# Kernel tuning notes

Hardware: AMD Instinct MI355X
Metric: run time of the kernel (lower is better)

## Reference

```python
import jax, jax.numpy as jnp
import numpy as np

# MLA dims (DeepSeek-V2-Lite-class)
B, S, D = 2, 2048, 2048
H = 16
NOPE, ROPE, VD = 128, 64, 128   # qk_nope_head_dim, qk_rope_head_dim, v_head_dim
KV_RANK, Q_RANK = 512, 1536
EPS = 1e-6
THETA = 10000.0


def setup_inputs() -> dict:
    key = jax.random.key(0)
    ks = jax.random.split(key, 8)

    def init(k, shape, fan_in):
        return jax.random.normal(k, shape, jnp.float32) * (fan_in ** -0.5)

    return {
        "x": jax.random.normal(ks[0], (B, S, D), jnp.float32),
        "w_dq": init(ks[1], (D, Q_RANK), D),
        "q_a_norm": jnp.ones((Q_RANK,), jnp.float32),
        "w_uq": init(ks[2], (Q_RANK, H * (NOPE + ROPE)), Q_RANK),
        "w_dkv": init(ks[3], (D, KV_RANK + ROPE), D),
        "kv_a_norm": jnp.ones((KV_RANK,), jnp.float32),
        "w_ukv": init(ks[4], (KV_RANK, H * (NOPE + VD)), KV_RANK),
        "w_o": init(ks[5], (H * VD, D), H * VD),
    }


def _rmsnorm(x, w):
    return x * jax.lax.rsqrt(jnp.mean(x * x, axis=-1, keepdims=True) + EPS) * w


def _rope(x):
    # x: [B, S, H', d] -> rotary on last dim (half-split style)
    d = x.shape[-1]
    inv = 1.0 / (THETA ** (jnp.arange(0, d, 2, dtype=jnp.float32) / d))
    ang = jnp.arange(x.shape[1], dtype=jnp.float32)[:, None] * inv[None, :]  # [S, d/2]
    cos = jnp.cos(ang)[None, :, None, :]
    sin = jnp.sin(ang)[None, :, None, :]
    x1, x2 = jnp.split(x, 2, axis=-1)
    return jnp.concatenate([x1 * cos - x2 * sin, x2 * cos + x1 * sin], axis=-1)


def reference(x, w_dq, q_a_norm, w_uq, w_dkv, kv_a_norm, w_ukv, w_o):
    # --- low-rank Q projection ---
    q = _rmsnorm(x @ w_dq, q_a_norm) @ w_uq          # [B,S,H*(NOPE+ROPE)]
    q = q.reshape(B, S, H, NOPE + ROPE)
    q_nope, q_pe = q[..., :NOPE], q[..., NOPE:]

    # --- latent (compressed) KV projection + shared decoupled-RoPE key ---
    ckv = x @ w_dkv                                   # [B,S,KV_RANK+ROPE]
    c_kv, k_pe = ckv[..., :KV_RANK], ckv[..., KV_RANK:]
    kv = (_rmsnorm(c_kv, kv_a_norm) @ w_ukv).reshape(B, S, H, NOPE + VD)
    k_nope, v = kv[..., :NOPE], kv[..., NOPE:]

    # --- decoupled RoPE on rope dims only ---
    q_pe = _rope(q_pe)                                # [B,S,H,ROPE]
    k_pe = _rope(k_pe[:, :, None, :])                 # [B,S,1,ROPE] shared across heads

    qf = jnp.concatenate([q_nope, q_pe], axis=-1)     # [B,S,H,NOPE+ROPE]
    kf = jnp.concatenate([k_nope, jnp.broadcast_to(k_pe, (B, S, H, ROPE))], axis=-1)

    # --- scaled dot-product attention with causal mask ---
    scale = 1.0 / jnp.sqrt(jnp.float32(NOPE + ROPE))
    scores = jnp.einsum("bqhd,bkhd->bhqk", qf * scale, kf)  # [B,H,S,S]
    causal = jnp.tril(jnp.ones((S, S), bool))
    scores = jnp.where(causal[None, None], scores, -1e9)
    w = jax.nn.softmax(scores, axis=-1)
    o = jnp.einsum("bhqk,bkhd->bqhd", w, v).reshape(B, S, H * VD)
    return o @ w_o                                    # [B,S,D]
```

## Files before the change

### kernel.cpp

```cpp
#include <hip/hip_runtime.h>
#include <hip/hip_bf16.h>
#include <math.h>

#define BB 2
#define SS 2048
#define DDIM 2048
#define HH 16
#define NOPE 128
#define ROPE_D 64
#define VD 128
#define KVR 512
#define QR 1536
#define EPSF 1e-6f
#define THETA 10000.0f
#define MR (BB*SS)

typedef unsigned short u16;
typedef unsigned int u32;
typedef __attribute__((ext_vector_type(8))) short bf8_t;
typedef __attribute__((ext_vector_type(4))) float f4_t;

__device__ inline u16 f2b(float f) {
    __hip_bfloat16 h = __float2bfloat16(f);
    return __builtin_bit_cast(u16, h);
}

#define GLD16(g, l) __builtin_amdgcn_global_load_lds( \
    (const __attribute__((address_space(1))) u32*)(g), \
    (__attribute__((address_space(3))) u32*)(l), 16, 0, 0)

#define MFMA16(a,b,c) __builtin_amdgcn_mfma_f32_16x16x32_bf16((a),(b),(c),0,0,0)

__device__ inline void cstore(float* p, float v) { *p = v; }
__device__ inline void cstore(u16* p, float v)   { *p = f2b(v); }

__global__ void cvt_bf16_k(const float* __restrict__ in, u16* __restrict__ out, int n4) {
    int i = blockIdx.x * 256 + threadIdx.x;
    if (i < n4) {
        float4 v = ((const float4*)in)[i];
        u16* o = out + (size_t)i * 4;
        o[0] = f2b(v.x); o[1] = f2b(v.y); o[2] = f2b(v.z); o[3] = f2b(v.w);
    }
}

__global__ void transpose_bf16_k(const float* __restrict__ W, u16* __restrict__ WT,
                                 int K, int N, int Npad) {
    __shared__ float t[32][33];
    int n0 = blockIdx.x * 32, k0 = blockIdx.y * 32;
    int tx = threadIdx.x, ty = threadIdx.y;
    for (int i = ty; i < 32; i += 8) {
        int n = n0 + tx;
        t[i][tx] = (n < N) ? W[(size_t)(k0 + i) * N + n] : 0.f;
    }
    __syncthreads();
    for (int i = ty; i < 32; i += 8) {
        int n = n0 + i;
        if (n < Npad) WT[(size_t)n * K + k0 + tx] = f2b(t[tx][i]);
    }
}

template <typename TO>
__global__ __launch_bounds__(256, 2)
void gemm_mfma(const u16* __restrict__ A, const u16* __restrict__ BT,
               TO* __restrict__ C, int K, int Nreal) {
    __shared__ u16 lA[128 * 32];
    __shared__ u16 lB[128 * 32];
    const int tid = threadIdx.x;
    const int w = tid >> 6, lane = tid & 63;
    const int quad = lane >> 4, col = lane & 15;
    const int wm = (w >> 1) * 64, wn = (w & 1) * 64;
    const int bm = blockIdx.y * 128, bn = blockIdx.x * 128;
    const int srow = lane >> 2;
    const int scol = (lane & 3) * 8;
    f4_t acc[4][4] = {};
    for (int k0 = 0; k0 < K; k0 += 32) {
        __syncthreads();
        #pragma unroll
        for (int cc = 0; cc < 2; cc++) {
            int c = 2 * w + cc;
            int row = c * 16 + srow;
            GLD16(A  + (size_t)(bm + row) * K + k0 + scol, (char*)lA + c * 1024);
            GLD16(BT + (size_t)(bn + row) * K + k0 + scol, (char*)lB + c * 1024);
        }
        __syncthreads();
        bf8_t af[4], bf[4];
        #pragma unroll
        for (int i = 0; i < 4; i++) {
            af[i] = *(const bf8_t*)(lA + (wm + i * 16 + col) * 32 + quad * 8);
            bf[i] = *(const bf8_t*)(lB + (wn + i * 16 + col) * 32 + quad * 8);
        }
        #pragma unroll
        for (int mi = 0; mi < 4; mi++)
            #pragma unroll
            for (int ni = 0; ni < 4; ni++)
                acc[mi][ni] = MFMA16(af[mi], bf[ni], acc[mi][ni]);
    }
    #pragma unroll
    for (int mi = 0; mi < 4; mi++)
        #pragma unroll
        for (int ni = 0; ni < 4; ni++) {
            int n = bn + wn + ni * 16 + col;
            if (n < Nreal) {
                #pragma unroll
                for (int r = 0; r < 4; r++) {
                    int m = bm + wm + mi * 16 + quad * 4 + r;
                    cstore(C + (size_t)m * Nreal + n, acc[mi][ni][r]);
                }
            }
        }
}

__global__ void rmsnorm_bf16_k(const float* __restrict__ in, int istride, int ncols,
                               const float* __restrict__ wt, u16* __restrict__ out, int ostride) {
    __shared__ float red[256];
    int row = blockIdx.x, tid = threadIdx.x;
    const float* rp = in + (size_t)row * istride;
    float s = 0.f;
    for (int c = tid; c < ncols; c += 256) { float v = rp[c]; s += v * v; }
    red[tid] = s;
    __syncthreads();
    for (int off = 128; off > 0; off >>= 1) {
        if (tid < off) red[tid] += red[tid + off];
        __syncthreads();
    }
    float sc = rsqrtf(red[0] / (float)ncols + EPSF);
    u16* op = out + (size_t)row * ostride;
    for (int c = tid; c < ncols; c += 256) op[c] = f2b(rp[c] * sc * wt[c]);
}

__global__ void rope_q_k(const float* __restrict__ q, u16* __restrict__ qb) {
    int idx = blockIdx.x;
    int pos = (idx >> 4) & (SS - 1);
    const float* src = q + (size_t)idx * 192;
    u16* dst = qb + (size_t)idx * 192;
    int t = threadIdx.x;
    dst[t]      = f2b(src[t]);
    dst[t + 64] = f2b(src[t + 64]);
    if (t < 32) {
        float inv = powf(THETA, -(float)t * (1.0f / 32.0f));
        float ang = (float)pos * inv;
        float cs, sn; sincosf(ang, &sn, &cs);
        float x1 = src[128 + t], x2 = src[160 + t];
        dst[128 + t] = f2b(x1 * cs - x2 * sn);
        dst[160 + t] = f2b(x2 * cs + x1 * sn);
    }
}

__global__ void rope_kpe_k(const float* __restrict__ ckv, u16* __restrict__ kpe) {
    int row = blockIdx.x;
    int pos = row & (SS - 1);
    int t = threadIdx.x;
    float inv = powf(THETA, -(float)t * (1.0f / 32.0f));
    float ang = (float)pos * inv;
    float cs, sn; sincosf(ang, &sn, &cs);
    const float* pe = ckv + (size_t)row * 576 + 512;
    float x1 = pe[t], x2 = pe[t + 32];
    kpe[(size_t)row * 64 + t]      = f2b(x1 * cs - x2 * sn);
    kpe[(size_t)row * 64 + 32 + t] = f2b(x2 * cs + x1 * sn);
}

__global__ __launch_bounds__(256, 2)
void attn_mfma(const u16* __restrict__ qb, const u16* __restrict__ kvb,
               const u16* __restrict__ kpe, u16* __restrict__ ob) {
    __shared__ u16 lK[64 * 200];
    __shared__ u16 lV[128 * 72];
    __shared__ u16 lP[4 * 16 * 72];
    const int tid = threadIdx.x, w = tid >> 6, lane = tid & 63;
    const int quad = lane >> 4, col = lane & 15;
    const int bh = blockIdx.x, b = bh >> 4, h = bh & 15;
    const int qt = 31 - (int)blockIdx.y;
    const int tok0 = b * SS;
    bf8_t qf[6];
    {
        int qtok = tok0 + qt * 64 + w * 16 + col;
        const u16* qp = qb + ((size_t)qtok * HH + h) * 192 + quad * 8;
        #pragma unroll
        for (int kc = 0; kc < 6; kc++) qf[kc] = *(const bf8_t*)(qp + kc * 32);
    }
    f4_t o[8] = {};
    float mrow[4] = {-1e30f, -1e30f, -1e30f, -1e30f};
    float lrow[4] = {0.f, 0.f, 0.f, 0.f};
    const float SCL = 0.07216878364870322f * 1.4426950408889634f;
    u16* pw = lP + w * 16 * 72;
    for (int kt = 0; kt <= qt; kt++) {
        int ktok = tok0 + kt * 64;
        __syncthreads();
        for (int c = w; c < 25; c += 4) {
            int o_b = c * 1024 + lane * 16;
            int row = o_b / 400;
            int ro  = o_b - row * 400;
            const u16* src;
            if (ro < 256)      src = kvb + ((size_t)(ktok + row) * HH + h) * 256 + (ro >> 1);
            else if (ro < 384) src = kpe + (size_t)(ktok + row) * 64 + ((ro - 256) >> 1);
            else               src = kpe;
            GLD16(src, (char*)lK + c * 1024);
        }
        #pragma unroll
        for (int i = 0; i < 4; i++) {
            int dv8 = w + i * 4;
            const u16* vp = kvb + ((size_t)(ktok + lane) * HH + h) * 256 + 128 + dv8 * 8;
            bf8_t vv = *(const bf8_t*)vp;
            #pragma unroll
            for (int j = 0; j < 8; j++) lV[(dv8 * 8 + j) * 72 + lane] = (u16)vv[j];
        }
        __syncthreads();
        f4_t s[4] = {};
        #pragma unroll
        for (int kc = 0; kc < 6; kc++) {
            #pragma unroll
            for (int t = 0; t < 4; t++) {
                bf8_t kf = *(const bf8_t*)(lK + (t * 16 + col) * 200 + kc * 32 + quad * 8);
                s[t] = MFMA16(qf[kc], kf, s[t]);
            }
        }
        float sm[4] = {-1e30f, -1e30f, -1e30f, -1e30f};
        #pragma unroll
        for (int t = 0; t < 4; t++) {
            int kg = kt * 64 + t * 16 + col;
            #pragma unroll
            for (int r = 0; r < 4; r++) {
                int qg = qt * 64 + w * 16 + quad * 4 + r;
                float v = (kg <= qg) ? s[t][r] * SCL : -1e30f;
                s[t][r] = v;
                sm[r] = fmaxf(sm[r], v);
            }
        }
        #pragma unroll
        for (int off = 1; off < 16; off <<= 1)
            #pragma unroll
            for (int r = 0; r < 4; r++) sm[r] = fmaxf(sm[r], __shfl_xor(sm[r], off));
        float al[4];
        #pragma unroll
        for (int r = 0; r < 4; r++) {
            float mn = fmaxf(mrow[r], sm[r]);
            al[r] = exp2f(mrow[r] - mn);
            mrow[r] = mn;
        }
        float rs[4] = {0.f, 0.f, 0.f, 0.f};
        #pragma unroll
        for (int t = 0; t < 4; t++)
            #pragma unroll
            for (int r = 0; r < 4; r++) {
                float p = exp2f(s[t][r] - mrow[r]);
                s[t][r] = p;
                rs[r] += p;
            }
        #pragma unroll
        for (int off = 1; off < 16; off <<= 1)
            #pragma unroll
            for (int r = 0; r < 4; r++) rs[r] += __shfl_xor(rs[r], off);
        #pragma unroll
        for (int r = 0; r < 4; r++) lrow[r] = lrow[r] * al[r] + rs[r];
        #pragma unroll
        for (int n = 0; n < 8; n++)
            #pragma unroll
            for (int r = 0; r < 4; r++) o[n][r] *= al[r];
        #pragma unroll
        for (int t = 0; t < 4; t++)
            #pragma unroll
            for (int r = 0; r < 4; r++)
                pw[(quad * 4 + r) * 72 + t * 16 + col] = f2b(s[t][r]);
        #pragma unroll
        for (int kc2 = 0; kc2 < 2; kc2++) {
            bf8_t pf = *(const bf8_t*)(pw + col * 72 + kc2 * 32 + quad * 8);
            #pragma unroll
            for (int n = 0; n < 8; n++) {
                bf8_t vf = *(const bf8_t*)(lV + (n * 16 + col) * 72 + kc2 * 32 + quad * 8);
                o[n] = MFMA16(pf, vf, o[n]);
            }
        }
    }
    #pragma unroll
    for (int n = 0; n < 8; n++)
        #pragma unroll
        for (int r = 0; r < 4; r++) {
            int qtok = tok0 + qt * 64 + w * 16 + quad * 4 + r;
            float v = o[n][r] / lrow[r];
            ob[((size_t)qtok * HH + h) * 128 + n * 16 + col] = f2b(v);
        }
}

extern "C" void kernel_launch(void* const* d_in, const int* in_sizes, int n_in,
                              void* d_out, int out_size, void* d_ws, size_t ws_size,
                              hipStream_t stream) {
    const float* x        = (const float*)d_in[0];
    const float* w_dq     = (const float*)d_in[1];
    const float* q_a_norm = (const float*)d_in[2];
    const float* w_uq     = (const float*)d_in[3];
    const float* w_dkv    = (const float*)d_in[4];
    const float* kv_a_nrm = (const float*)d_in[5];
    const float* w_ukv    = (const float*)d_in[6];
    const float* w_o      = (const float*)d_in[7];
    float* out = (float*)d_out;

    char* ws = (char*)d_ws;
    const size_t MB = 1024 * 1024;
    u16*   xb    = (u16*)(ws);
    u16*   wT    = (u16*)(ws + 16 * MB);
    float* qlat  = (float*)(ws + 25 * MB);
    u16*   qlb   = (u16*)(ws + 49 * MB);
    float* qf32  = (float*)(ws + 61 * MB);
    u16*   qbuf  = (u16*)(ws + 25 * MB);
    float* ckv   = (float*)(ws + 49 * MB);
    u16*   ckvnb = (u16*)(ws + 61 * MB);
    u16*   kpeb  = (u16*)(ws + 61 * MB + 4 * MB);
    u16*   kvb   = (u16*)(ws + 61 * MB + 5 * MB);
    u16*   aob   = (u16*)(ws);

    cvt_bf16_k<<<(MR * DDIM / 4 + 255) / 256, 256, 0, stream>>>(x, xb, MR * DDIM / 4);
    transpose_bf16_k<<<dim3(1536 / 32, 2048 / 32), dim3(32, 8), 0, stream>>>(w_dq, wT, 2048, 1536, 1536);
    gemm_mfma<float><<<dim3(1536 / 128, MR / 128), 256, 0, stream>>>(xb, wT, qlat, 2048, 1536);
    rmsnorm_bf16_k<<<MR, 256, 0, stream>>>(qlat, QR, QR, q_a_norm, qlb, QR);
    transpose_bf16_k<<<dim3(3072 / 32, 1536 / 32), dim3(32, 8), 0, stream>>>(w_uq, wT, 1536, 3072, 3072);
    gemm_mfma<float><<<dim3(3072 / 128, MR / 128), 256, 0, stream>>>(qlb, wT, qf32, 1536, 3072);
    rope_q_k<<<MR * HH, 64, 0, stream>>>(qf32, qbuf);
    transpose_bf16_k<<<dim3(640 / 32, 2048 / 32), dim3(32, 8), 0, stream>>>(w_dkv, wT, 2048, 576, 640);
    gemm_mfma<float><<<dim3(640 / 128, MR / 128), 256, 0, stream>>>(xb, wT, ckv, 2048, 576);
    rmsnorm_bf16_k<<<MR, 256, 0, stream>>>(ckv, 576, KVR, kv_a_nrm, ckvnb, KVR);
    rope_kpe_k<<<MR, 32, 0, stream>>>(ckv, kpeb);
    transpose_bf16_k<<<dim3(4096 / 32, 512 / 32), dim3(32, 8), 0, stream>>>(w_ukv, wT, 512, 4096, 4096);
    gemm_mfma<u16><<<dim3(4096 / 128, MR / 128), 256, 0, stream>>>(ckvnb, wT, kvb, 512, 4096);
    attn_mfma<<<dim3(32, 32), 256, 0, stream>>>(qbuf, kvb, kpeb, aob);
    transpose_bf16_k<<<dim3(2048 / 32, 2048 / 32), dim3(32, 8), 0, stream>>>(w_o, wT, 2048, 2048, 2048);
    gemm_mfma<float><<<dim3(2048 / 128, MR / 128), 256, 0, stream>>>(aob, wT, out, 2048, 2048);
}
```

Baseline: 540.2 us.

## Fuse prep kernels, merge down-projections, fold RoPE into GEMM, pair causal attention tiles

All weight transposes and the x conversion now run in one prep kernel. The Q and KV down-projection GEMMs are merged into a single GEMM with bf16 output, and RMSNorm reads bf16. Q RoPE and the softmax scale are folded into the up-projection GEMM epilogue. The attention grid is halved, with each block handling a short and a long causal query tile to balance work. It also skips masked diagonal MFMAs, hoists load offsets, packs the V transpose with perm, and raises occupancy to 3 blocks. Storing intermediates in bf16 adds precision risk.

```diff
diff --git a/kernel.cpp b/kernel.cpp
--- a/kernel.cpp
+++ b/kernel.cpp
@@ -2,18 +2,12 @@
 #include <hip/hip_bf16.h>
 #include <math.h>
 
-#define BB 2
 #define SS 2048
-#define DDIM 2048
 #define HH 16
-#define NOPE 128
-#define ROPE_D 64
-#define VD 128
-#define KVR 512
-#define QR 1536
 #define EPSF 1e-6f
-#define THETA 10000.0f
-#define MR (BB*SS)
+#define MR 4096
+#define L2T 13.287712379549449f
+#define ASCL (0.07216878364870322f * 1.4426950408889634f)
 
 typedef unsigned short u16;
 typedef unsigned int u32;
@@ -24,6 +18,10 @@
     __hip_bfloat16 h = __float2bfloat16(f);
     return __builtin_bit_cast(u16, h);
 }
+__device__ inline float b2f(u16 x) {
+    u32 v = (u32)x << 16;
+    return __builtin_bit_cast(float, v);
+}
 
 #define GLD16(g, l) __builtin_amdgcn_global_load_lds( \
     (const __attribute__((address_space(1))) u32*)(g), \
@@ -31,38 +29,46 @@
 
 #define MFMA16(a,b,c) __builtin_amdgcn_mfma_f32_16x16x32_bf16((a),(b),(c),0,0,0)
 
-__device__ inline void cstore(float* p, float v) { *p = v; }
-__device__ inline void cstore(u16* p, float v)   { *p = f2b(v); }
-
-__global__ void cvt_bf16_k(const float* __restrict__ in, u16* __restrict__ out, int n4) {
-    int i = blockIdx.x * 256 + threadIdx.x;
-    if (i < n4) {
-        float4 v = ((const float4*)in)[i];
-        u16* o = out + (size_t)i * 4;
-        o[0] = f2b(v.x); o[1] = f2b(v.y); o[2] = f2b(v.z); o[3] = f2b(v.w);
-    }
-}
-
-__global__ void transpose_bf16_k(const float* __restrict__ W, u16* __restrict__ WT,
-                                 int K, int N, int Npad) {
-    __shared__ float t[32][33];
-    int n0 = blockIdx.x * 32, k0 = blockIdx.y * 32;
-    int tx = threadIdx.x, ty = threadIdx.y;
+__global__ void prep_k(const float* __restrict__ x, u16* __restrict__ xb,
+                       const float* __restrict__ w_dq, const float* __restrict__ w_dkv,
+                       const float* __restrict__ w_uq, const float* __restrict__ w_ukv,
+                       const float* __restrict__ w_o,
+                       u16* __restrict__ wT1, u16* __restrict__ wTuq,
+                       u16* __restrict__ wTukv, u16* __restrict__ wTo) {
+    __shared__ float tt[32][33];
+    int blk = blockIdx.x, tid = threadIdx.x;
+    if (blk < 8192) {
+        int i = blk * 256 + tid;
+        float4 v = ((const float4*)x)[i];
+        ushort4 o;
+        o.x = f2b(v.x); o.y = f2b(v.y); o.z = f2b(v.z); o.w = f2b(v.w);
+        *(ushort4*)(xb + (size_t)i * 4) = o;
+        return;
+    }
+    blk -= 8192;
+    const float* W; u16* dst; int K, N, Npad, nx;
+    if (blk < 3072)       { W = w_dq;  dst = wT1;                      K = 2048; N = 1536; Npad = 1536; nx = 48; }
+    else if (blk < 4352)  { blk -= 3072; W = w_dkv; dst = wT1 + (size_t)1536 * 2048; K = 2048; N = 576;  Npad = 640;  nx = 20; }
+    else if (blk < 8960)  { blk -= 4352; W = w_uq;  dst = wTuq;        K = 1536; N = 3072; Npad = 3072; nx = 96; }
+    else if (blk < 11008) { blk -= 8960; W = w_ukv; dst = wTukv;       K = 512;  N = 4096; Npad = 4096; nx = 128; }
+    else                  { blk -= 11008; W = w_o;  dst = wTo;         K = 2048; N = 2048; Npad = 2048; nx = 64; }
+    int n0 = (blk % nx) * 32, k0 = (blk / nx) * 32;
+    int tx = tid & 31, ty = tid >> 5;
     for (int i = ty; i < 32; i += 8) {
         int n = n0 + tx;
-        t[i][tx] = (n < N) ? W[(size_t)(k0 + i) * N + n] : 0.f;
+        tt[i][tx] = (n < N) ? W[(size_t)(k0 + i) * N + n] : 0.f;
     }
     __syncthreads();
     for (int i = ty; i < 32; i += 8) {
         int n = n0 + i;
-        if (n < Npad) WT[(size_t)n * K + k0 + tx] = f2b(t[tx][i]);
-    }
-}
-
-template <typename TO>
+        if (n < Npad) dst[(size_t)n * K + k0 + tx] = f2b(tt[tx][i]);
+    }
+}
+
+template <int MODE>
 __global__ __launch_bounds__(256, 2)
 void gemm_mfma(const u16* __restrict__ A, const u16* __restrict__ BT,
-               TO* __restrict__ C, int K, int Nreal) {
+               void* __restrict__ Cv, int K, int N) {
     __shared__ u16 lA[128 * 32];
     __shared__ u16 lB[128 * 32];
     const int tid = threadIdx.x;
@@ -95,189 +101,291 @@
             for (int ni = 0; ni < 4; ni++)
                 acc[mi][ni] = MFMA16(af[mi], bf[ni], acc[mi][ni]);
     }
-    #pragma unroll
-    for (int mi = 0; mi < 4; mi++)
-        #pragma unroll
-        for (int ni = 0; ni < 4; ni++) {
-            int n = bn + wn + ni * 16 + col;
-            if (n < Nreal) {
+    if (MODE == 0) {
+        float* C = (float*)Cv;
+        #pragma unroll
+        for (int mi = 0; mi < 4; mi++)
+            #pragma unroll
+            for (int ni = 0; ni < 4; ni++) {
+                int n = bn + wn + ni * 16 + col;
                 #pragma unroll
                 for (int r = 0; r < 4; r++) {
                     int m = bm + wm + mi * 16 + quad * 4 + r;
-                    cstore(C + (size_t)m * Nreal + n, acc[mi][ni][r]);
+                    C[(size_t)m * N + n] = acc[mi][ni][r];
+                }
+            }
+    } else if (MODE == 1) {
+        u16* C = (u16*)Cv;
+        #pragma unroll
+        for (int mi = 0; mi < 4; mi++)
+            #pragma unroll
+            for (int ni = 0; ni < 4; ni++) {
+                int n = bn + wn + ni * 16 + col;
+                #pragma unroll
+                for (int r = 0; r < 4; r++) {
+                    int m = bm + wm + mi * 16 + quad * 4 + r;
+                    C[(size_t)m * N + n] = f2b(acc[mi][ni][r]);
+                }
+            }
+    } else {
+        u16* C = (u16*)Cv;
+        int span = ((bn + wn) >> 6) % 3;
+        if (span < 2) {
+            #pragma unroll
+            for (int mi = 0; mi < 4; mi++)
+                #pragma unroll
+                for (int ni = 0; ni < 4; ni++) {
+                    int n = bn + wn + ni * 16 + col;
+                    #pragma unroll
+                    for (int r = 0; r < 4; r++) {
+                        int m = bm + wm + mi * 16 + quad * 4 + r;
+                        C[(size_t)m * N + n] = f2b(acc[mi][ni][r] * ASCL);
+                    }
+                }
+        } else {
+            #pragma unroll
+            for (int ni = 0; ni < 2; ni++) {
+                int e = ni * 16 + col;
+                float inv = exp2f(-(float)e * (L2T / 32.0f));
+                #pragma unroll
+                for (int mi = 0; mi < 4; mi++) {
+                    #pragma unroll
+                    for (int r = 0; r < 4; r++) {
+                        int m = bm + wm + mi * 16 + quad * 4 + r;
+                        int pos = m & (SS - 1);
+                        float ang = (float)pos * inv;
+                        float cs, sn; sincosf(ang, &sn, &cs);
+                        float x1 = acc[mi][ni][r], x2 = acc[mi][ni + 2][r];
+                        int n = bn + wn + ni * 16 + col;
+                        C[(size_t)m * N + n]      = f2b((x1 * cs - x2 * sn) * ASCL);
+                        C[(size_t)m * N + n + 32] = f2b((x2 * cs + x1 * sn) * ASCL);
+                    }
                 }
             }
         }
-}
-
-__global__ void rmsnorm_bf16_k(const float* __restrict__ in, int istride, int ncols,
-                               const float* __restrict__ wt, u16* __restrict__ out, int ostride) {
+    }
+}
+
+__global__ void rmsq_k(const u16* __restrict__ C1, const float* __restrict__ wt,
+                       u16* __restrict__ qlb) {
     __shared__ float red[256];
     int row = blockIdx.x, tid = threadIdx.x;
-    const float* rp = in + (size_t)row * istride;
+    const ushort4* rp = (const ushort4*)(C1 + (size_t)row * 2176);
     float s = 0.f;
-    for (int c = tid; c < ncols; c += 256) { float v = rp[c]; s += v * v; }
+    for (int i = tid; i < 384; i += 256) {
+        ushort4 u = rp[i];
+        float a = b2f(u.x), b = b2f(u.y), c = b2f(u.z), d = b2f(u.w);
+        s += a * a + b * b + c * c + d * d;
+    }
     red[tid] = s;
     __syncthreads();
     for (int off = 128; off > 0; off >>= 1) {
         if (tid < off) red[tid] += red[tid + off];
         __syncthreads();
     }
-    float sc = rsqrtf(red[0] / (float)ncols + EPSF);
-    u16* op = out + (size_t)row * ostride;
-    for (int c = tid; c < ncols; c += 256) op[c] = f2b(rp[c] * sc * wt[c]);
-}
-
-__global__ void rope_q_k(const float* __restrict__ q, u16* __restrict__ qb) {
-    int idx = blockIdx.x;
-    int pos = (idx >> 4) & (SS - 1);
-    const float* src = q + (size_t)idx * 192;
-    u16* dst = qb + (size_t)idx * 192;
-    int t = threadIdx.x;
-    dst[t]      = f2b(src[t]);
-    dst[t + 64] = f2b(src[t + 64]);
-    if (t < 32) {
-        float inv = powf(THETA, -(float)t * (1.0f / 32.0f));
+    float sc = rsqrtf(red[0] * (1.0f / 1536.0f) + EPSF);
+    ushort4* op = (ushort4*)(qlb + (size_t)row * 1536);
+    const float4* wv = (const float4*)wt;
+    for (int i = tid; i < 384; i += 256) {
+        ushort4 u = rp[i];
+        float4 ww = wv[i];
+        ushort4 o;
+        o.x = f2b(b2f(u.x) * sc * ww.x);
+        o.y = f2b(b2f(u.y) * sc * ww.y);
+        o.z = f2b(b2f(u.z) * sc * ww.z);
+        o.w = f2b(b2f(u.w) * sc * ww.w);
+        op[i] = o;
+    }
+}
+
+__global__ void rmskv_rope_k(const u16* __restrict__ C1, const float* __restrict__ wt,
+                             u16* __restrict__ ckvnb, u16* __restrict__ kpeb) {
+    __shared__ float red[256];
+    int row = blockIdx.x, tid = threadIdx.x;
+    const u16* base = C1 + (size_t)row * 2176 + 1536;
+    if (tid < 32) {
+        int t = tid;
+        float x1 = b2f(base[512 + t]), x2 = b2f(base[544 + t]);
+        int pos = row & (SS - 1);
+        float inv = exp2f(-(float)t * (L2T / 32.0f));
         float ang = (float)pos * inv;
         float cs, sn; sincosf(ang, &sn, &cs);
-        float x1 = src[128 + t], x2 = src[160 + t];
-        dst[128 + t] = f2b(x1 * cs - x2 * sn);
-        dst[160 + t] = f2b(x2 * cs + x1 * sn);
-    }
-}
-
-__global__ void rope_kpe_k(const float* __restrict__ ckv, u16* __restrict__ kpe) {
-    int row = blockIdx.x;
-    int pos = row & (SS - 1);
-    int t = threadIdx.x;
-    float inv = powf(THETA, -(float)t * (1.0f / 32.0f));
-    float ang = (float)pos * inv;
-    float cs, sn; sincosf(ang, &sn, &cs);
-    const float* pe = ckv + (size_t)row * 576 + 512;
-    float x1 = pe[t], x2 = pe[t + 32];
-    kpe[(size_t)row * 64 + t]      = f2b(x1 * cs - x2 * sn);
-    kpe[(size_t)row * 64 + 32 + t] = f2b(x2 * cs + x1 * sn);
-}
-
-__global__ __launch_bounds__(256, 2)
+        kpeb[(size_t)row * 64 + t]      = f2b(x1 * cs - x2 * sn);
+        kpeb[(size_t)row * 64 + 32 + t] = f2b(x2 * cs + x1 * sn);
+    }
+    const ushort4* rp = (const ushort4*)base;
+    float s = 0.f;
+    if (tid < 128) {
+        ushort4 u = rp[tid];
+        float a = b2f(u.x), b = b2f(u.y), c = b2f(u.z), d = b2f(u.w);
+        s = a * a + b * b + c * c + d * d;
+    }
+    red[tid] = s;
+    __syncthreads();
+    for (int off = 128; off > 0; off >>= 1) {
+        if (tid < off) red[tid] += red[tid + off];
+        __syncthreads();
+    }
+    float sc = rsqrtf(red[0] * (1.0f / 512.0f) + EPSF);
+    if (tid < 128) {
+        ushort4 u = rp[tid];
+        float4 ww = ((const float4*)wt)[tid];
+        ushort4 o;
+        o.x = f2b(b2f(u.x) * sc * ww.x);
+        o.y = f2b(b2f(u.y) * sc * ww.y);
+        o.z = f2b(b2f(u.z) * sc * ww.z);
+        o.w = f2b(b2f(u.w) * sc * ww.w);
+        ((ushort4*)(ckvnb + (size_t)row * 512))[tid] = o;
+    }
+}
+
+__global__ __launch_bounds__(256, 3)
 void attn_mfma(const u16* __restrict__ qb, const u16* __restrict__ kvb,
                const u16* __restrict__ kpe, u16* __restrict__ ob) {
     __shared__ u16 lK[64 * 200];
     __shared__ u16 lV[128 * 72];
-    __shared__ u16 lP[4 * 16 * 72];
+    __shared__ u16 lP[4 * 16 * 80];
     const int tid = threadIdx.x, w = tid >> 6, lane = tid & 63;
     const int quad = lane >> 4, col = lane & 15;
     const int bh = blockIdx.x, b = bh >> 4, h = bh & 15;
-    const int qt = 31 - (int)blockIdx.y;
     const int tok0 = b * SS;
-    bf8_t qf[6];
-    {
-        int qtok = tok0 + qt * 64 + w * 16 + col;
-        const u16* qp = qb + ((size_t)qtok * HH + h) * 192 + quad * 8;
-        #pragma unroll
-        for (int kc = 0; kc < 6; kc++) qf[kc] = *(const bf8_t*)(qp + kc * 32);
-    }
-    f4_t o[8] = {};
-    float mrow[4] = {-1e30f, -1e30f, -1e30f, -1e30f};
-    float lrow[4] = {0.f, 0.f, 0.f, 0.f};
-    const float SCL = 0.07216878364870322f * 1.4426950408889634f;
-    u16* pw = lP + w * 16 * 72;
-    for (int kt = 0; kt <= qt; kt++) {
-        int ktok = tok0 + kt * 64;
-        __syncthreads();
-        for (int c = w; c < 25; c += 4) {
-            int o_b = c * 1024 + lane * 16;
-            int row = o_b / 400;
-            int ro  = o_b - row * 400;
-            const u16* src;
-            if (ro < 256)      src = kvb + ((size_t)(ktok + row) * HH + h) * 256 + (ro >> 1);
-            else if (ro < 384) src = kpe + (size_t)(ktok + row) * 64 + ((ro - 256) >> 1);
-            else               src = kpe;
-            GLD16(src, (char*)lK + c * 1024);
+    int offE[7], isKV[7];
+    #pragma unroll
+    for (int jj = 0; jj < 7; jj++) {
+        int c = w + 4 * jj;
+        int o_b = c * 1024 + lane * 16;
+        int row = o_b / 400;
+        int ro = o_b - row * 400;
+        if (ro < 256)      { offE[jj] = (row * 16 + h) * 256 + (ro >> 1); isKV[jj] = 1; }
+        else if (ro < 384) { offE[jj] = row * 64 + ((ro - 256) >> 1);     isKV[jj] = 0; }
+        else               { offE[jj] = 0;                                 isKV[jj] = 0; }
+    }
+    const int kp2 = lane & 31, dh = lane >> 5;
+    u16* pw = lP + w * 16 * 80;
+
+    for (int ph = 0; ph < 2; ph++) {
+        const int qt = ph ? (31 - (int)blockIdx.y) : (int)blockIdx.y;
+        bf8_t qf[6];
+        {
+            int qtok = tok0 + qt * 64 + w * 16 + col;
+            const u16* qp = qb + ((size_t)qtok * HH + h) * 192 + quad * 8;
+            #pragma unroll
+            for (int kc = 0; kc < 6; kc++) qf[kc] = *(const bf8_t*)(qp + kc * 32);
         }
-        #pragma unroll
-        for (int i = 0; i < 4; i++) {
-            int dv8 = w + i * 4;
-            const u16* vp = kvb + ((size_t)(ktok + lane) * HH + h) * 256 + 128 + dv8 * 8;
-            bf8_t vv = *(const bf8_t*)vp;
-            #pragma unroll
-            for (int j = 0; j < 8; j++) lV[(dv8 * 8 + j) * 72 + lane] = (u16)vv[j];
+        f4_t o[8] = {};
+        float mrow[4] = {-1e30f, -1e30f, -1e30f, -1e30f};
+        float lrow[4] = {0.f, 0.f, 0.f, 0.f};
+        for (int kt = 0; kt <= qt; kt++) {
+            int ktok = tok0 + kt * 64;
+            __syncthreads();
+            #pragma unroll
+            for (int jj = 0; jj < 7; jj++) {
+                int c = w + 4 * jj;
+                if (c < 25) {
+                    const u16* src = isKV[jj] ? kvb + (size_t)ktok * 4096 + offE[jj]
+                                              : kpe + (size_t)ktok * 64   + offE[jj];
+                    GLD16(src, (char*)lK + c * 1024);
+                }
+            }
+            #pragma unroll
+            for (int i = 0; i < 2; i++) {
+                int dv8 = w * 4 + dh * 2 + i;
+                const u16* v0 = kvb + ((size_t)(ktok + 2 * kp2) * HH + h) * 256 + 128 + dv8 * 8;
+                uint4 a4 = *(const uint4*)v0;
+                uint4 b4 = *(const uint4*)(v0 + 4096);
+                u32 av[4] = {a4.x, a4.y, a4.z, a4.w};
+                u32 bv[4] = {b4.x, b4.y, b4.z, b4.w};
+                u32* dst = (u32*)lV + (size_t)(dv8 * 8) * 36 + kp2;
+                #pragma unroll
+                for (int t = 0; t < 4; t++) {
+                    u32 lo = __builtin_amdgcn_perm(bv[t], av[t], 0x05040100u);
+                    u32 hi = __builtin_amdgcn_perm(bv[t], av[t], 0x07060302u);
+                    dst[(2 * t) * 36]     = lo;
+                    dst[(2 * t + 1) * 36] = hi;
+                }
+            }
+            __syncthreads();
+            bool diag = (kt == qt);
+            f4_t s[4] = {};
+            #pragma unroll
+            for (int t = 0; t < 4; t++) {
+                if (!diag || t <= w) {
+                    #pragma unroll
+                    for (int kc = 0; kc < 6; kc++) {
+                        bf8_t kf = *(const bf8_t*)(lK + (t * 16 + col) * 200 + kc * 32 + quad * 8);
+                        s[t] = MFMA16(qf[kc], kf, s[t]);
+                    }
+                }
+            }
+            if (diag) {
+                #pragma unroll
+                for (int t = 0; t < 4; t++) {
+                    int kg = t * 16 + col;
+                    #pragma unroll
+                    for (int r = 0; r < 4; r++) {
+                        int qg = w * 16 + quad * 4 + r;
+                        if (kg > qg) s[t][r] = -1e30f;
+                    }
+                }
+            }
+            float sm[4] = {-1e30f, -1e30f, -1e30f, -1e30f};
+            #pragma unroll
+            for (int t = 0; t < 4; t++)
+                #pragma unroll
+                for (int r = 0; r < 4; r++) sm[r] = fmaxf(sm[r], s[t][r]);
+            #pragma unroll
+            for (int off = 1; off < 16; off <<= 1)
+                #pragma unroll
+                for (int r = 0; r < 4; r++) sm[r] = fmaxf(sm[r], __shfl_xor(sm[r], off));
+            float al[4];
+            #pragma unroll
+            for (int r = 0; r < 4; r++) {
+                float mn = fmaxf(mrow[r], sm[r]);
+                al[r] = exp2f(mrow[r] - mn);
+                mrow[r] = mn;
+            }
+            float rs[4] = {0.f, 0.f, 0.f, 0.f};
+            #pragma unroll
+            for (int t = 0; t < 4; t++)
+                #pragma unroll
+                for (int r = 0; r < 4; r++) {
+                    float p = exp2f(s[t][r] - mrow[r]);
+                    s[t][r] = p;
+                    rs[r] += p;
+                }
+            #pragma unroll
+            for (int off = 1; off < 16; off <<= 1)
+                #pragma unroll
+                for (int r = 0; r < 4; r++) rs[r] += __shfl_xor(rs[r], off);
+            #pragma unroll
+            for (int r = 0; r < 4; r++) lrow[r] = lrow[r] * al[r] + rs[r];
+            #pragma unroll
+            for (int n = 0; n < 8; n++)
+                #pragma unroll
+                for (int r = 0; r < 4; r++) o[n][r] *= al[r];
+            #pragma unroll
+            for (int t = 0; t < 4; t++)
+                #pragma unroll
+                for (int r = 0; r < 4; r++)
+                    pw[(quad * 4 + r) * 80 + t * 16 + col] = f2b(s[t][r]);
+            #pragma unroll
+            for (int kc2 = 0; kc2 < 2; kc2++) {
+                bf8_t pf = *(const bf8_t*)(pw + col * 80 + kc2 * 32 + quad * 8);
+                #pragma unroll
+                for (int n = 0; n < 8; n++) {
+                    bf8_t vf = *(const bf8_t*)(lV + (n * 16 + col) * 72 + kc2 * 32 + quad * 8);
+                    o[n] = MFMA16(pf, vf, o[n]);
+                }
+            }
         }
-        __syncthreads();
-        f4_t s[4] = {};
-        #pragma unroll
-        for (int kc = 0; kc < 6; kc++) {
-            #pragma unroll
-            for (int t = 0; t < 4; t++) {
-                bf8_t kf = *(const bf8_t*)(lK + (t * 16 + col) * 200 + kc * 32 + quad * 8);
-                s[t] = MFMA16(qf[kc], kf, s[t]);
-            }
-        }
-        float sm[4] = {-1e30f, -1e30f, -1e30f, -1e30f};
-        #pragma unroll
-        for (int t = 0; t < 4; t++) {
-            int kg = kt * 64 + t * 16 + col;
+        #pragma unroll
+        for (int n = 0; n < 8; n++)
             #pragma unroll
             for (int r = 0; r < 4; r++) {
-                int qg = qt * 64 + w * 16 + quad * 4 + r;
-                float v = (kg <= qg) ? s[t][r] * SCL : -1e30f;
-                s[t][r] = v;
-                sm[r] = fmaxf(sm[r], v);
-            }
-        }
-        #pragma unroll
-        for (int off = 1; off < 16; off <<= 1)
-            #pragma unroll
-            for (int r = 0; r < 4; r++) sm[r] = fmaxf(sm[r], __shfl_xor(sm[r], off));
-        float al[4];
-        #pragma unroll
-        for (int r = 0; r < 4; r++) {
-            float mn = fmaxf(mrow[r], sm[r]);
-            al[r] = exp2f(mrow[r] - mn);
-            mrow[r] = mn;
-        }
-        float rs[4] = {0.f, 0.f, 0.f, 0.f};
-        #pragma unroll
-        for (int t = 0; t < 4; t++)
-            #pragma unroll
-            for (int r = 0; r < 4; r++) {
-                float p = exp2f(s[t][r] - mrow[r]);
-                s[t][r] = p;
-                rs[r] += p;
-            }
-        #pragma unroll
-        for (int off = 1; off < 16; off <<= 1)
-            #pragma unroll
-            for (int r = 0; r < 4; r++) rs[r] += __shfl_xor(rs[r], off);
-        #pragma unroll
-        for (int r = 0; r < 4; r++) lrow[r] = lrow[r] * al[r] + rs[r];
-        #pragma unroll
-        for (int n = 0; n < 8; n++)
-            #pragma unroll
-            for (int r = 0; r < 4; r++) o[n][r] *= al[r];
-        #pragma unroll
-        for (int t = 0; t < 4; t++)
-            #pragma unroll
-            for (int r = 0; r < 4; r++)
-                pw[(quad * 4 + r) * 72 + t * 16 + col] = f2b(s[t][r]);
-        #pragma unroll
-        for (int kc2 = 0; kc2 < 2; kc2++) {
-            bf8_t pf = *(const bf8_t*)(pw + col * 72 + kc2 * 32 + quad * 8);
-            #pragma unroll
-            for (int n = 0; n < 8; n++) {
-                bf8_t vf = *(const bf8_t*)(lV + (n * 16 + col) * 72 + kc2 * 32 + quad * 8);
-                o[n] = MFMA16(pf, vf, o[n]);
-            }
-        }
-    }
-    #pragma unroll
-    for (int n = 0; n < 8; n++)
-        #pragma unroll
-        for (int r = 0; r < 4; r++) {
-            int qtok = tok0 + qt * 64 + w * 16 + quad * 4 + r;
-            float v = o[n][r] / lrow[r];
-            ob[((size_t)qtok * HH + h) * 128 + n * 16 + col] = f2b(v);
-        }
+                int qtok = tok0 + qt * 64 + w * 16 + quad * 4 + r;
+                ob[((size_t)qtok * HH + h) * 128 + n * 16 + col] = f2b(o[n][r] / lrow[r]);
+            }
+    }
 }
 
 extern "C" void kernel_launch(void* const* d_in, const int* in_sizes, int n_in,
@@ -295,32 +403,26 @@
 
     char* ws = (char*)d_ws;
     const size_t MB = 1024 * 1024;
-    u16*   xb    = (u16*)(ws);
-    u16*   wT    = (u16*)(ws + 16 * MB);
-    float* qlat  = (float*)(ws + 25 * MB);
-    u16*   qlb   = (u16*)(ws + 49 * MB);
-    float* qf32  = (float*)(ws + 61 * MB);
-    u16*   qbuf  = (u16*)(ws + 25 * MB);
-    float* ckv   = (float*)(ws + 49 * MB);
-    u16*   ckvnb = (u16*)(ws + 61 * MB);
-    u16*   kpeb  = (u16*)(ws + 61 * MB + 4 * MB);
-    u16*   kvb   = (u16*)(ws + 61 * MB + 5 * MB);
-    u16*   aob   = (u16*)(ws);
-
-    cvt_bf16_k<<<(MR * DDIM / 4 + 255) / 256, 256, 0, stream>>>(x, xb, MR * DDIM / 4);
-    transpose_bf16_k<<<dim3(1536 / 32, 2048 / 32), dim3(32, 8), 0, stream>>>(w_dq, wT, 2048, 1536, 1536);
-    gemm_mfma<float><<<dim3(1536 / 128, MR / 128), 256, 0, stream>>>(xb, wT, qlat, 2048, 1536);
-    rmsnorm_bf16_k<<<MR, 256, 0, stream>>>(qlat, QR, QR, q_a_norm, qlb, QR);
-    transpose_bf16_k<<<dim3(3072 / 32, 1536 / 32), dim3(32, 8), 0, stream>>>(w_uq, wT, 1536, 3072, 3072);
-    gemm_mfma<float><<<dim3(3072 / 128, MR / 128), 256, 0, stream>>>(qlb, wT, qf32, 1536, 3072);
-    rope_q_k<<<MR * HH, 64, 0, stream>>>(qf32, qbuf);
-    transpose_bf16_k<<<dim3(640 / 32, 2048 / 32), dim3(32, 8), 0, stream>>>(w_dkv, wT, 2048, 576, 640);
-    gemm_mfma<float><<<dim3(640 / 128, MR / 128), 256, 0, stream>>>(xb, wT, ckv, 2048, 576);
-    rmsnorm_bf16_k<<<MR, 256, 0, stream>>>(ckv, 576, KVR, kv_a_nrm, ckvnb, KVR);
-    rope_kpe_k<<<MR, 32, 0, stream>>>(ckv, kpeb);
-    transpose_bf16_k<<<dim3(4096 / 32, 512 / 32), dim3(32, 8), 0, stream>>>(w_ukv, wT, 512, 4096, 4096);
-    gemm_mfma<u16><<<dim3(4096 / 128, MR / 128), 256, 0, stream>>>(ckvnb, wT, kvb, 512, 4096);
-    attn_mfma<<<dim3(32, 32), 256, 0, stream>>>(qbuf, kvb, kpeb, aob);
-    transpose_bf16_k<<<dim3(2048 / 32, 2048 / 32), dim3(32, 8), 0, stream>>>(w_o, wT, 2048, 2048, 2048);
-    gemm_mfma<float><<<dim3(2048 / 128, MR / 128), 256, 0, stream>>>(aob, wT, out, 2048, 2048);
-}
+    u16* xb    = (u16*)(ws);
+    u16* wT1   = (u16*)(ws + 17 * MB);
+    u16* wTuq  = (u16*)(ws + 26 * MB);
+    u16* wTukv = (u16*)(ws + 36 * MB);
+    u16* wTo   = (u16*)(ws + 41 * MB);
+    u16* C1    = (u16*)(ws + 50 * MB);
+    u16* qlb   = (u16*)(ws + 68 * MB);
+    u16* qbuf  = (u16*)(ws + 81 * MB);
+    u16* ckvnb = (u16*)(ws + 106 * MB);
+    u16* kpeb  = (u16*)(ws + 110 * MB);
+    u16* kvb   = (u16*)(ws + 111 * MB);
+    u16* aob   = xb;
+
+    prep_k<<<23296, 256, 0, stream>>>(x, xb, w_dq, w_dkv, w_uq, w_ukv, w_o,
+                                      wT1, wTuq, wTukv, wTo);
+    gemm_mfma<1><<<dim3(17, 32), 256, 0, stream>>>(xb, wT1, C1, 2048, 2176);
+    rmsq_k<<<MR, 256, 0, stream>>>(C1, q_a_norm, qlb);
+    gemm_mfma<2><<<dim3(24, 32), 256, 0, stream>>>(qlb, wTuq, qbuf, 1536, 3072);
+    rmskv_rope_k<<<MR, 256, 0, stream>>>(C1, kv_a_nrm, ckvnb, kpeb);
+    gemm_mfma<1><<<dim3(32, 32), 256, 0, stream>>>(ckvnb, wTukv, kvb, 512, 4096);
+    attn_mfma<<<dim3(32, 16), 256, 0, stream>>>(qbuf, kvb, kpeb, aob);
+    gemm_mfma<0><<<dim3(16, 32), 256, 0, stream>>>(aob, wTo, out, 2048, 2048);
+}
```

Result: faster. 462.0 us (-14.5%).
